# Optimization experiments

Measured on AMD Instinct MI355X. Metric: run time of the kernel, lower is better.

The kernel has to match this reference:

```python
import jax, jax.numpy as jnp
import numpy as np
import math

DIM = 512
NUM_HEADS = 8
DIM_HEAD = DIM // NUM_HEADS


def normalized_coords(h, w):
    # (h*w, 2) with (x, y) in [0, 1]
    y = jnp.linspace(0.0, 1.0, h)
    x = jnp.linspace(0.0, 1.0, w)
    yg, xg = jnp.meshgrid(y, x, indexing='ij')
    return jnp.stack([xg.ravel(), yg.ravel()], axis=-1)


def rotate_half(x):
    dh = x.shape[-1] // 2
    return jnp.concatenate([-x[..., dh:], x[..., :dh]], axis=-1)


def apply_rope(t, coords):
    # t: (n, heads, seq, dim_head); coords: (seq, 2) (identical across batch)
    dim_half = t.shape[-1] // 2
    freq = 1.0 / (10000.0 ** (jnp.arange(dim_half, dtype=jnp.float32) / dim_half))
    ang_x = coords[:, 0:1] * freq  # (seq, dim_half)
    ang_y = coords[:, 1:2] * freq
    ang = jnp.concatenate([ang_x, ang_y], axis=-1)  # (seq, dim_head)
    cos, sin = jnp.cos(ang), jnp.sin(ang)
    return t * cos + rotate_half(t) * sin


def setup_inputs() -> dict:
    key = jax.random.key(0)
    ks = jax.random.split(key, 12)
    n, Np, d, H, W = 4, 1024, DIM, 64, 64
    s = 0.02
    return {
        'local_feat': jax.random.normal(ks[0], (n, Np, d), jnp.float32),
        'global_feat': jax.random.normal(ks[1], (n, d, H, W), jnp.float32),
        'Wq': jax.random.normal(ks[2], (d, d), jnp.float32) * s,
        'bq': jnp.zeros((d,), jnp.float32),
        'Wk': jax.random.normal(ks[3], (d, d), jnp.float32) * s,
        'bk': jnp.zeros((d,), jnp.float32),
        'Wv': jax.random.normal(ks[4], (d, d), jnp.float32) * s,
        'bv': jnp.zeros((d,), jnp.float32),
        'Wg': jax.random.normal(ks[5], (d, 2 * d), jnp.float32) * s,
        'bg': jnp.zeros((d,), jnp.float32),
        'Wo': jax.random.normal(ks[6], (d, d), jnp.float32) * s,
        'bo': jnp.zeros((d,), jnp.float32),
    }


def reference(local_feat, global_feat, Wq, bq, Wk, bk, Wv, bv, Wg, bg, Wo, bo):
    n, Np, d = local_feat.shape
    _, _, H, W = global_feat.shape
    h, dh = NUM_HEADS, DIM_HEAD
    gf = global_feat.reshape(n, d, H * W).transpose(0, 2, 1)  # (n, HW, d)

    P = int(math.isqrt(Np))
    local_coords = normalized_coords(P, P)      # (Np, 2)
    global_coords = normalized_coords(H, W)     # (HW, 2)

    def proj(x, Wt, b):
        return x @ Wt.T + b

    Q = proj(local_feat, Wq, bq).reshape(n, Np, h, dh).transpose(0, 2, 1, 3)
    K = proj(gf, Wk, bk).reshape(n, H * W, h, dh).transpose(0, 2, 1, 3)
    V = proj(gf, Wv, bv).reshape(n, H * W, h, dh).transpose(0, 2, 1, 3)

    Q = apply_rope(Q, local_coords)
    K = apply_rope(K, global_coords)

    scores = jnp.einsum('bhqd,bhkd->bhqk', Q, K) / math.sqrt(dh)
    attn = jax.nn.softmax(scores, axis=-1)
    ao = jnp.einsum('bhqk,bhkd->bhqd', attn, V)
    ao = ao.transpose(0, 2, 1, 3).reshape(n, Np, d)

    gate = jax.nn.sigmoid(jnp.concatenate([local_feat, ao], axis=-1) @ Wg.T + bg)
    enhanced = local_feat + gate * ao
    return enhanced @ Wo.T + bo
```

## Files before the change

### kernel.cpp

```cpp
#include <hip/hip_runtime.h>
#include <hip/hip_bf16.h>
#include <cstdint>

typedef __hip_bfloat16 BF;
typedef unsigned short ushort_t;
typedef __attribute__((ext_vector_type(8))) __bf16 bf16x8;
typedef __attribute__((ext_vector_type(4))) float f32x4;

__device__ __forceinline__ float b2f(BF x) { return __bfloat162float(x); }
__device__ __forceinline__ unsigned short f2bu(float f) {
  union { BF b; unsigned short u; } c; c.b = __float2bfloat16(f); return c.u;
}
__device__ __forceinline__ float rdE(const void* p, size_t i, bool f32) {
  return f32 ? ((const float*)p)[i] : __bfloat162float(((const BF*)p)[i]);
}
__device__ __forceinline__ void rd16(const void* p, size_t i, bool f32, ushort_t* out) {
  if (f32) {
    const float* fp = (const float*)p + i;
#pragma unroll
    for (int j = 0; j < 16; j += 4) {
      float4 v = *(const float4*)(fp + j);
      out[j] = f2bu(v.x); out[j + 1] = f2bu(v.y);
      out[j + 2] = f2bu(v.z); out[j + 3] = f2bu(v.w);
    }
  } else {
    const uint4* up = (const uint4*)((const BF*)p + i);
    *(uint4*)&out[0] = up[0];
    *(uint4*)&out[8] = up[1];
  }
}

__global__ void detect_k(const unsigned short* __restrict__ x, int* __restrict__ flag) {
  __shared__ int cnt;
  if (threadIdx.x == 0) cnt = 0;
  __syncthreads();
  int c = 0;
  for (int i = threadIdx.x; i < 4096; i += 256) {
    int e = (x[i] >> 7) & 0xFF;
    if (e >= 0x86) c++;
  }
  if (c) atomicAdd(&cnt, c);
  __syncthreads();
  if (threadIdx.x == 0) *flag = (cnt > 64) ? 1 : 0;
}

template <int MODE>
__global__ __launch_bounds__(256) void mgemm_k(
    const void* __restrict__ Aext, const BF* __restrict__ Aint,
    const void* __restrict__ Bw, const void* __restrict__ Bw2,
    const void* __restrict__ biasv, const void* __restrict__ bias2,
    BF* __restrict__ outInt, BF* __restrict__ outInt2,
    void* __restrict__ outExt, int Kdim, const int* __restrict__ flagp) {
  const bool f32 = (*flagp != 0);
  const int tid = threadIdx.x;
  const int w = tid >> 6, lane = tid & 63;
  const int quad = lane >> 4, l16 = lane & 15;

  if constexpr (MODE == 5) {
    __shared__ __align__(16) ushort_t smem[2][128][72];
    auto As = smem[0];
    auto Bs = smem[1];
    const int wm = w >> 1, wn = w & 1;
    const int g = blockIdx.x;
    const int a = g & 7, y = (g >> 3) & 7, bidx = g >> 6;
    const int m0 = ((bidx << 1) | (a & 1)) * 128;
    const int n0 = y * 128;
    const int bz = a >> 1;

    f32x4 acc[4][4] = {};
    for (int k0 = 0; k0 < Kdim; k0 += 64) {
      __syncthreads();
#pragma unroll
      for (int u = 0; u < 2; ++u) {
        int unit = tid + u * 256;
        int k = unit >> 3, mg = unit & 7;
        int ksw = k ^ (8 * (mg & 3));
        size_t base = (size_t)bz * 512 * 4096 + (size_t)(k0 + k) * 4096 + m0 + mg * 16;
        ushort_t vals[16];
        rd16(Aext, base, f32, vals);
#pragma unroll
        for (int j = 0; j < 16; ++j) As[mg * 16 + j][ksw] = vals[j];
      }
#pragma unroll
      for (int u = 0; u < 2; ++u) {
        int unit = tid + u * 256;
        int row = unit >> 2, cg = unit & 3;
        const void* bsrc = (n0 >= 512) ? Bw2 : Bw;
        size_t nrow = (n0 >= 512) ? (n0 - 512 + row) : (n0 + row);
        ushort_t vals[16];
        rd16(bsrc, nrow * Kdim + k0 + cg * 16, f32, vals);
        *(uint4*)&Bs[row][cg * 16] = *(uint4*)&vals[0];
        *(uint4*)&Bs[row][cg * 16 + 8] = *(uint4*)&vals[8];
      }
      __syncthreads();
#pragma unroll
      for (int kc = 0; kc < 2; ++kc) {
        bf16x8 af[4], bfv[4];
#pragma unroll
        for (int i = 0; i < 4; ++i) {
          int col = (kc * 32 + quad * 8) ^ (8 * (i & 3));
          af[i] = *(const bf16x8*)&As[wm * 64 + i * 16 + l16][col];
          bfv[i] = *(const bf16x8*)&Bs[wn * 64 + i * 16 + l16][kc * 32 + quad * 8];
        }
#pragma unroll
        for (int mt = 0; mt < 4; ++mt)
#pragma unroll
          for (int nt = 0; nt < 4; ++nt)
            acc[mt][nt] = __builtin_amdgcn_mfma_f32_16x16x32_bf16(af[mt], bfv[nt], acc[mt][nt], 0, 0, 0);
      }
    }
    if (n0 < 512) {
      const int head = (n0 + wn * 64) >> 6;
#pragma unroll
      for (int mt = 0; mt < 4; ++mt)
#pragma unroll
        for (int r = 0; r < 4; ++r) {
          int pg = m0 + wm * 64 + mt * 16 + quad * 4 + r;
          float x = (float)(pg & 63) * (1.f / 63.f);
          float yy = (float)(pg >> 6) * (1.f / 63.f);
          size_t base = (((size_t)bz * 8 + head) * 4096 + pg) * 64;
#pragma unroll
          for (int j = 0; j < 2; ++j) {
            int c0 = j * 16 + l16;
            float t0 = acc[mt][j][r] + rdE(biasv, head * 64 + c0, f32);
            float t1 = acc[mt][j + 2][r] + rdE(biasv, head * 64 + c0 + 32, f32);
            float fr = __expf((float)c0 * (-9.210340371976184f / 32.f));
            float ax = x * fr, ay = yy * fr;
            outInt[base + c0] = __float2bfloat16(t0 * __cosf(ax) - t1 * __sinf(ax));
            outInt[base + c0 + 32] = __float2bfloat16(t1 * __cosf(ay) + t0 * __sinf(ay));
          }
        }
    } else {
      const int n0v = n0 - 512;
      __syncthreads();
      ushort_t (*T)[136] = (ushort_t(*)[136]) & smem[0][0][0];
#pragma unroll
      for (int mt = 0; mt < 4; ++mt)
#pragma unroll
        for (int nt = 0; nt < 4; ++nt)
#pragma unroll
          for (int r = 0; r < 4; ++r) {
            int n_l = wn * 64 + nt * 16 + l16;
            int m_l = wm * 64 + mt * 16 + quad * 4 + r;
            T[n_l][m_l] = f2bu(acc[mt][nt][r] + rdE(bias2, n0v + n_l, f32));
          }
      __syncthreads();
      int row = tid >> 1, half = tid & 1;
      size_t gbase = (((size_t)bz * 8 + (n0v >> 6) + (row >> 6)) * 64 + (row & 63)) * 4096 +
                     m0 + half * 64;
      uint4* dst = (uint4*)(outInt2 + gbase);
      const uint4* src = (const uint4*)&T[row][half * 64];
#pragma unroll
      for (int j = 0; j < 8; ++j) dst[j] = src[j];
    }
  } else {
    __shared__ __align__(16) ushort_t As[64][72];
    __shared__ __align__(16) ushort_t Bs[64][72];
    const int m0 = blockIdx.x * 64, n0 = blockIdx.y * 64;

    f32x4 acc[4] = {};
    for (int k0 = 0; k0 < Kdim; k0 += 64) {
      __syncthreads();
      {
        int row = tid >> 2, cg = tid & 3;
        int kg = k0 + cg * 16;
        ushort_t vals[16];
        if constexpr (MODE == 3) {
          if (kg < 512) {
            rd16(Aext, (size_t)(m0 + row) * 512 + kg, f32, vals);
          } else {
            const uint4* p = (const uint4*)(Aint + (size_t)(m0 + row) * 512 + (kg - 512));
            *(uint4*)&vals[0] = p[0]; *(uint4*)&vals[8] = p[1];
          }
        } else if constexpr (MODE == 4) {
          const uint4* p = (const uint4*)(Aint + (size_t)(m0 + row) * 512 + kg);
          *(uint4*)&vals[0] = p[0]; *(uint4*)&vals[8] = p[1];
        } else {
          rd16(Aext, (size_t)(m0 + row) * Kdim + kg, f32, vals);
        }
        *(uint4*)&As[row][cg * 16] = *(uint4*)&vals[0];
        *(uint4*)&As[row][cg * 16 + 8] = *(uint4*)&vals[8];
        ushort_t bv[16];
        rd16(Bw, (size_t)(n0 + row) * Kdim + kg, f32, bv);
        *(uint4*)&Bs[row][cg * 16] = *(uint4*)&bv[0];
        *(uint4*)&Bs[row][cg * 16 + 8] = *(uint4*)&bv[8];
      }
      __syncthreads();
#pragma unroll
      for (int kc = 0; kc < 2; ++kc) {
        bf16x8 af = *(const bf16x8*)&As[w * 16 + l16][kc * 32 + quad * 8];
#pragma unroll
        for (int nt = 0; nt < 4; ++nt) {
          bf16x8 bfv = *(const bf16x8*)&Bs[nt * 16 + l16][kc * 32 + quad * 8];
          acc[nt] = __builtin_amdgcn_mfma_f32_16x16x32_bf16(af, bfv, acc[nt], 0, 0, 0);
        }
      }
    }

    if constexpr (MODE == 0) {
      const int head = n0 >> 6;
#pragma unroll
      for (int r = 0; r < 4; ++r) {
        int mg = m0 + w * 16 + quad * 4 + r;
        int bb = mg >> 10, qi = mg & 1023;
        float x = (float)(qi & 31) * (1.f / 31.f);
        float y = (float)(qi >> 5) * (1.f / 31.f);
        size_t base = (((size_t)bb * 8 + head) * 1024 + qi) * 64;
#pragma unroll
        for (int j = 0; j < 2; ++j) {
          int c0 = j * 16 + l16;
          float t0 = acc[j][r] + rdE(biasv, head * 64 + c0, f32);
          float t1 = acc[j + 2][r] + rdE(biasv, head * 64 + c0 + 32, f32);
          float fr = __expf((float)c0 * (-9.210340371976184f / 32.f));
          float ax = x * fr, ay = y * fr;
          outInt[base + c0] = __float2bfloat16(t0 * __cosf(ax) - t1 * __sinf(ax));
          outInt[base + c0 + 32] = __float2bfloat16(t1 * __cosf(ay) + t0 * __sinf(ay));
        }
      }
    } else if constexpr (MODE == 3) {
#pragma unroll
      for (int r = 0; r < 4; ++r) {
        int mg = m0 + w * 16 + quad * 4 + r;
#pragma unroll
        for (int nt = 0; nt < 4; ++nt) {
          int ng = n0 + nt * 16 + l16;
          size_t idx = (size_t)mg * 512 + ng;
          float g = 1.f / (1.f + __expf(-(acc[nt][r] + rdE(biasv, ng, f32))));
          outInt[idx] = __float2bfloat16(rdE(Aext, idx, f32) + g * b2f(Aint[idx]));
        }
      }
    } else {
#pragma unroll
      for (int r = 0; r < 4; ++r) {
        int mg = m0 + w * 16 + quad * 4 + r;
#pragma unroll
        for (int nt = 0; nt < 4; ++nt) {
          int ng = n0 + nt * 16 + l16;
          size_t idx = (size_t)mg * 512 + ng;
          float v = acc[nt][r] + rdE(biasv, ng, f32);
          if (f32) ((float*)outExt)[idx] = v;
          else ((BF*)outExt)[idx] = __float2bfloat16(v);
        }
      }
    }
  }
}

template <int NS>
__global__ __launch_bounds__(256) void attn_k(const BF* __restrict__ Q,
                                              const BF* __restrict__ K,
                                              const BF* __restrict__ VT,
                                              BF* __restrict__ AO,
                                              BF* __restrict__ Opart,
                                              float* __restrict__ lpart) {
  __shared__ __align__(16) ushort_t Ks[64][72];
  __shared__ __align__(16) ushort_t VTs[64][72];
  __shared__ __align__(16) ushort_t Ps[4][32][72];

  const int tid = threadIdx.x;
  const int w = tid >> 6, lane = tid & 63;
  const int quad = lane >> 4, l16 = lane & 15;

  const int g = blockIdx.x;
  const int bh = g & 31;
  const int qt = (g >> 5) & 7;
  const int ks = g >> 8;
  const int b = bh >> 3, h = bh & 7;
  const int q0 = qt * 128 + w * 32;
  const int kspan = 4096 / NS, kbase = ks * kspan;

  bf16x8 qa[2][2];
#pragma unroll
  for (int qs = 0; qs < 2; ++qs) {
    const BF* qp = Q + (((size_t)bh << 10) + q0 + qs * 16 + l16) * 64 + quad * 8;
#pragma unroll
    for (int hh = 0; hh < 2; ++hh) {
      bf16x8 t = *(const bf16x8*)(qp + 32 * hh);
#pragma unroll
      for (int j = 0; j < 8; ++j) t[j] = (__bf16)(0.1803368801111f * (float)t[j]);
      qa[qs][hh] = t;
    }
  }

  const BF* Kp = K + (size_t)bh * 4096 * 64;
  const BF* VTp = VT + (size_t)bh * 64 * 4096;

  f32x4 o[2][4] = {};
  float lp[2][4] = {};

  const int srow = tid >> 2, scol = (tid & 3) * 16;
  {
    const uint4* kp = (const uint4*)(Kp + (size_t)(kbase + srow) * 64 + scol);
    const uint4* vp = (const uint4*)(VTp + (size_t)srow * 4096 + kbase + scol);
    uint4 a = kp[0], bb = kp[1], c = vp[0], d = vp[1];
    *(uint4*)&Ks[srow][scol] = a;  *(uint4*)&Ks[srow][scol + 8] = bb;
    *(uint4*)&VTs[srow][scol] = c; *(uint4*)&VTs[srow][scol + 8] = d;
  }

  for (int c0 = kbase; c0 < kbase + kspan; c0 += 64) {
    __syncthreads();
    uint4 nk0, nk1, nv0, nv1;
    const bool more = (c0 + 64 < kbase + kspan);
    if (more) {
      const uint4* kp = (const uint4*)(Kp + (size_t)(c0 + 64 + srow) * 64 + scol);
      const uint4* vp = (const uint4*)(VTp + (size_t)srow * 4096 + c0 + 64 + scol);
      nk0 = kp[0]; nk1 = kp[1]; nv0 = vp[0]; nv1 = vp[1];
    }

#pragma unroll
    for (int ct = 0; ct < 4; ++ct) {
      bf16x8 kb0 = *(const bf16x8*)&Ks[ct * 16 + l16][quad * 8];
      bf16x8 kb1 = *(const bf16x8*)&Ks[ct * 16 + l16][32 + quad * 8];
#pragma unroll
      for (int qs = 0; qs < 2; ++qs) {
        f32x4 s = {};
        s = __builtin_amdgcn_mfma_f32_16x16x32_bf16(qa[qs][0], kb0, s, 0, 0, 0);
        s = __builtin_amdgcn_mfma_f32_16x16x32_bf16(qa[qs][1], kb1, s, 0, 0, 0);
#pragma unroll
        for (int r = 0; r < 4; ++r) {
          float p = __builtin_exp2f(s[r]);
          lp[qs][r] += p;
          Ps[w][qs * 16 + quad * 4 + r][ct * 16 + l16] = f2bu(p);
        }
      }
    }

    bf16x8 pa[2][2];
#pragma unroll
    for (int qs = 0; qs < 2; ++qs) {
      pa[qs][0] = *(const bf16x8*)&Ps[w][qs * 16 + l16][quad * 8];
      pa[qs][1] = *(const bf16x8*)&Ps[w][qs * 16 + l16][32 + quad * 8];
    }
#pragma unroll
    for (int nt = 0; nt < 4; ++nt) {
      bf16x8 vb0 = *(const bf16x8*)&VTs[nt * 16 + l16][quad * 8];
      bf16x8 vb1 = *(const bf16x8*)&VTs[nt * 16 + l16][32 + quad * 8];
#pragma unroll
      for (int qs = 0; qs < 2; ++qs) {
        o[qs][nt] = __builtin_amdgcn_mfma_f32_16x16x32_bf16(pa[qs][0], vb0, o[qs][nt], 0, 0, 0);
        o[qs][nt] = __builtin_amdgcn_mfma_f32_16x16x32_bf16(pa[qs][1], vb1, o[qs][nt], 0, 0, 0);
      }
    }

    __syncthreads();
    if (more) {
      *(uint4*)&Ks[srow][scol] = nk0;  *(uint4*)&Ks[srow][scol + 8] = nk1;
      *(uint4*)&VTs[srow][scol] = nv0; *(uint4*)&VTs[srow][scol + 8] = nv1;
    }
  }

#pragma unroll
  for (int qs = 0; qs < 2; ++qs) {
    float invl[4];
#pragma unroll
    for (int r = 0; r < 4; ++r) {
      float v = lp[qs][r];
#pragma unroll
      for (int d = 1; d < 16; d <<= 1) v += __shfl_xor(v, d);
      if (NS == 1) invl[r] = 1.f / v;
      else if (l16 == 0)
        lpart[ks * 32768 + (bh << 10) + q0 + qs * 16 + quad * 4 + r] = v;
    }
#pragma unroll
    for (int nt = 0; nt < 4; ++nt)
#pragma unroll
      for (int r = 0; r < 4; ++r) {
        int qg = q0 + qs * 16 + quad * 4 + r;
        if (NS == 1) {
          AO[(((size_t)b << 10) + qg) * 512 + h * 64 + nt * 16 + l16] =
              __float2bfloat16(o[qs][nt][r] * invl[r]);
        } else {
          Opart[(size_t)ks * 2097152 + (((size_t)bh << 10) + qg) * 64 + nt * 16 + l16] =
              __float2bfloat16(o[qs][nt][r]);
        }
      }
  }
}

template <int NS>
__global__ __launch_bounds__(256) void reduce_k(const BF* __restrict__ Opart,
                                                const float* __restrict__ lpart,
                                                BF* __restrict__ AO) {
  int e0 = (blockIdx.x * 256 + threadIdx.x) * 4;
  int row = e0 >> 6, col = e0 & 63;
  float lsum = 0.f;
#pragma unroll
  for (int s = 0; s < NS; ++s) lsum += lpart[s * 32768 + row];
  float inv = 1.f / lsum;
  float acc[4] = {};
#pragma unroll
  for (int s = 0; s < NS; ++s) {
    uint2 u = *(const uint2*)((const ushort_t*)Opart + (size_t)s * 2097152 +
                              (size_t)row * 64 + col);
    const ushort_t* pu = (const ushort_t*)&u;
#pragma unroll
    for (int j = 0; j < 4; ++j)
      acc[j] += __uint_as_float((unsigned)pu[j] << 16);
  }
  ushort_t outv[4];
#pragma unroll
  for (int j = 0; j < 4; ++j) outv[j] = f2bu(acc[j] * inv);
  int bh = row >> 10, q = row & 1023, bb = bh >> 3, h = bh & 7;
  *(uint2*)(AO + (((size_t)bb << 10) + q) * 512 + h * 64 + col) = *(uint2*)outv;
}

extern "C" void kernel_launch(void* const* d_in, const int* in_sizes, int n_in,
                              void* d_out, int out_size, void* d_ws, size_t ws_size,
                              hipStream_t stream) {
  const void* local = d_in[0];
  const void* gfeat = d_in[1];
  const void* Wq = d_in[2];
  const void* bq = d_in[3];
  const void* Wk = d_in[4];
  const void* bk = d_in[5];
  const void* Wv = d_in[6];
  const void* bv = d_in[7];
  const void* Wg = d_in[8];
  const void* bg = d_in[9];
  const void* Wo = d_in[10];
  const void* bo = d_in[11];

  char* w = (char*)d_ws;
  int* flag = (int*)w;        w += 256;
  BF* Qb = (BF*)w;            w += (size_t)2097152 * 2;
  BF* Kb = (BF*)w;            w += (size_t)8388608 * 2;
  BF* VTb = (BF*)w;           w += (size_t)8388608 * 2;
  BF* AO = (BF*)w;            w += (size_t)2097152 * 2;
  BF* Opart = (BF*)w;
  size_t baseOff = (size_t)(w - (char*)d_ws);
  BF* ENH = Qb;

  int NS = 1;
  if (baseOff + 4 * (4194304 + 131072) <= ws_size) NS = 4;
  else if (baseOff + 2 * (4194304 + 131072) <= ws_size) NS = 2;
  float* lpart = (float*)(w + (size_t)NS * 4194304);

  dim3 blk(256);
  detect_k<<<dim3(1), blk, 0, stream>>>((const unsigned short*)local, flag);
  mgemm_k<0><<<dim3(64, 8, 1), blk, 0, stream>>>(local, nullptr, Wq, nullptr, bq, nullptr, Qb, nullptr, nullptr, 512, flag);
  mgemm_k<5><<<dim3(1024, 1, 1), blk, 0, stream>>>(gfeat, nullptr, Wk, Wv, bk, bv, Kb, VTb, nullptr, 512, flag);
  if (NS == 4) {
    attn_k<4><<<dim3(1024), blk, 0, stream>>>(Qb, Kb, VTb, AO, Opart, lpart);
    reduce_k<4><<<dim3(2048), blk, 0, stream>>>(Opart, lpart, AO);
  } else if (NS == 2) {
    attn_k<2><<<dim3(512), blk, 0, stream>>>(Qb, Kb, VTb, AO, Opart, lpart);
    reduce_k<2><<<dim3(2048), blk, 0, stream>>>(Opart, lpart, AO);
  } else {
    attn_k<1><<<dim3(256), blk, 0, stream>>>(Qb, Kb, VTb, AO, nullptr, nullptr);
  }
  mgemm_k<3><<<dim3(64, 8, 1), blk, 0, stream>>>(local, AO, Wg, nullptr, bg, nullptr, ENH, nullptr, nullptr, 1024, flag);
  mgemm_k<4><<<dim3(64, 8, 1), blk, 0, stream>>>(nullptr, ENH, Wo, nullptr, bo, nullptr, nullptr, nullptr, d_out, 512, flag);
}
```

Before: 293.7 us.

## Pre-transpose global features, fold Q scale into projection, transpose attention MFMAs

Adds a prep kernel that transposes global_feat into a row-major bf16 buffer, so the K/V projection GEMM loads A tiles as contiguous vectors instead of doing strided 16-element scatter writes into swizzled LDS. The softmax scale is folded into the Q projection epilogue, and the attention kernel swaps MFMA operand order so P is written to LDS with vector stores. Row sums now come from an MFMA against a ones vector instead of per-lane accumulation plus shuffles, and the output is written with packed vector stores. The cost is an extra kernel launch plus a 16 MB intermediate that shares workspace with Opart, and the NS=2 workspace check is adjusted to fit it.

```diff
diff --git a/kernel.cpp b/kernel.cpp
--- a/kernel.cpp
+++ b/kernel.cpp
@@ -44,6 +44,33 @@
   if (threadIdx.x == 0) *flag = (cnt > 64) ? 1 : 0;
 }
 
+__global__ __launch_bounds__(256) void prep_k(const void* __restrict__ gfeat,
+                                              BF* __restrict__ gfT,
+                                              const int* __restrict__ flagp) {
+  const bool f32 = (*flagp != 0);
+  __shared__ __align__(16) ushort_t T[64][72];
+  const int g = blockIdx.x;
+  const int bz = g & 3, mt = (g >> 2) & 63, kt = g >> 8;
+  const int t = threadIdx.x;
+  {
+    int krow = t >> 2, mg = t & 3;
+    ushort_t vals[16];
+    rd16(gfeat,
+         (size_t)bz * 512 * 4096 + (size_t)(kt * 64 + krow) * 4096 + mt * 64 + mg * 16,
+         f32, vals);
+#pragma unroll
+    for (int j = 0; j < 16; ++j) T[mg * 16 + j][krow] = vals[j];
+  }
+  __syncthreads();
+  int mrow = t >> 2, kg = t & 3;
+  uint4 a = *(const uint4*)&T[mrow][kg * 16];
+  uint4 b = *(const uint4*)&T[mrow][kg * 16 + 8];
+  size_t o = ((size_t)bz * 4096 + mt * 64 + mrow) * 512 + kt * 64 + kg * 16;
+  *(uint4*)&gfT[o] = a;
+  *(uint4*)&gfT[o + 8] = b;
+}
+
+#define QS 0.1803368801111f
 template <int MODE>
 __global__ __launch_bounds__(256) void mgemm_k(
     const void* __restrict__ Aext, const BF* __restrict__ Aint,
@@ -73,13 +100,11 @@
 #pragma unroll
       for (int u = 0; u < 2; ++u) {
         int unit = tid + u * 256;
-        int k = unit >> 3, mg = unit & 7;
-        int ksw = k ^ (8 * (mg & 3));
-        size_t base = (size_t)bz * 512 * 4096 + (size_t)(k0 + k) * 4096 + m0 + mg * 16;
-        ushort_t vals[16];
-        rd16(Aext, base, f32, vals);
-#pragma unroll
-        for (int j = 0; j < 16; ++j) As[mg * 16 + j][ksw] = vals[j];
+        int row = unit >> 2, cg = unit & 3;
+        const uint4* p = (const uint4*)(Aint + ((size_t)bz * 4096 + m0 + row) * 512 +
+                                        k0 + cg * 16);
+        *(uint4*)&As[row][cg * 16] = p[0];
+        *(uint4*)&As[row][cg * 16 + 8] = p[1];
       }
 #pragma unroll
       for (int u = 0; u < 2; ++u) {
@@ -98,8 +123,7 @@
         bf16x8 af[4], bfv[4];
 #pragma unroll
         for (int i = 0; i < 4; ++i) {
-          int col = (kc * 32 + quad * 8) ^ (8 * (i & 3));
-          af[i] = *(const bf16x8*)&As[wm * 64 + i * 16 + l16][col];
+          af[i] = *(const bf16x8*)&As[wm * 64 + i * 16 + l16][kc * 32 + quad * 8];
           bfv[i] = *(const bf16x8*)&Bs[wn * 64 + i * 16 + l16][kc * 32 + quad * 8];
         }
 #pragma unroll
@@ -213,8 +237,8 @@
           float t1 = acc[j + 2][r] + rdE(biasv, head * 64 + c0 + 32, f32);
           float fr = __expf((float)c0 * (-9.210340371976184f / 32.f));
           float ax = x * fr, ay = y * fr;
-          outInt[base + c0] = __float2bfloat16(t0 * __cosf(ax) - t1 * __sinf(ax));
-          outInt[base + c0 + 32] = __float2bfloat16(t1 * __cosf(ay) + t0 * __sinf(ay));
+          outInt[base + c0] = __float2bfloat16((t0 * __cosf(ax) - t1 * __sinf(ax)) * QS);
+          outInt[base + c0 + 32] = __float2bfloat16((t1 * __cosf(ay) + t0 * __sinf(ay)) * QS);
         }
       }
     } else if constexpr (MODE == 3) {
@@ -273,20 +297,18 @@
 #pragma unroll
   for (int qs = 0; qs < 2; ++qs) {
     const BF* qp = Q + (((size_t)bh << 10) + q0 + qs * 16 + l16) * 64 + quad * 8;
-#pragma unroll
-    for (int hh = 0; hh < 2; ++hh) {
-      bf16x8 t = *(const bf16x8*)(qp + 32 * hh);
-#pragma unroll
-      for (int j = 0; j < 8; ++j) t[j] = (__bf16)(0.1803368801111f * (float)t[j]);
-      qa[qs][hh] = t;
-    }
-  }
+    qa[qs][0] = *(const bf16x8*)qp;
+    qa[qs][1] = *(const bf16x8*)(qp + 32);
+  }
+  bf16x8 ones;
+#pragma unroll
+  for (int j = 0; j < 8; ++j) ones[j] = (__bf16)1.0f;
 
   const BF* Kp = K + (size_t)bh * 4096 * 64;
   const BF* VTp = VT + (size_t)bh * 64 * 4096;
 
   f32x4 o[2][4] = {};
-  float lp[2][4] = {};
+  f32x4 ol[2] = {};
 
   const int srow = tid >> 2, scol = (tid & 3) * 16;
   {
@@ -314,31 +336,27 @@
 #pragma unroll
       for (int qs = 0; qs < 2; ++qs) {
         f32x4 s = {};
-        s = __builtin_amdgcn_mfma_f32_16x16x32_bf16(qa[qs][0], kb0, s, 0, 0, 0);
-        s = __builtin_amdgcn_mfma_f32_16x16x32_bf16(qa[qs][1], kb1, s, 0, 0, 0);
-#pragma unroll
-        for (int r = 0; r < 4; ++r) {
-          float p = __builtin_exp2f(s[r]);
-          lp[qs][r] += p;
-          Ps[w][qs * 16 + quad * 4 + r][ct * 16 + l16] = f2bu(p);
-        }
-      }
-    }
-
-    bf16x8 pa[2][2];
+        s = __builtin_amdgcn_mfma_f32_16x16x32_bf16(kb0, qa[qs][0], s, 0, 0, 0);
+        s = __builtin_amdgcn_mfma_f32_16x16x32_bf16(kb1, qa[qs][1], s, 0, 0, 0);
+        ushort_t pv[4];
+#pragma unroll
+        for (int r = 0; r < 4; ++r) pv[r] = f2bu(__builtin_exp2f(s[r]));
+        *(uint2*)&Ps[w][qs * 16 + l16][ct * 16 + quad * 4] = *(uint2*)pv;
+      }
+    }
+
 #pragma unroll
     for (int qs = 0; qs < 2; ++qs) {
-      pa[qs][0] = *(const bf16x8*)&Ps[w][qs * 16 + l16][quad * 8];
-      pa[qs][1] = *(const bf16x8*)&Ps[w][qs * 16 + l16][32 + quad * 8];
-    }
-#pragma unroll
-    for (int nt = 0; nt < 4; ++nt) {
-      bf16x8 vb0 = *(const bf16x8*)&VTs[nt * 16 + l16][quad * 8];
-      bf16x8 vb1 = *(const bf16x8*)&VTs[nt * 16 + l16][32 + quad * 8];
-#pragma unroll
-      for (int qs = 0; qs < 2; ++qs) {
-        o[qs][nt] = __builtin_amdgcn_mfma_f32_16x16x32_bf16(pa[qs][0], vb0, o[qs][nt], 0, 0, 0);
-        o[qs][nt] = __builtin_amdgcn_mfma_f32_16x16x32_bf16(pa[qs][1], vb1, o[qs][nt], 0, 0, 0);
+      bf16x8 pa0 = *(const bf16x8*)&Ps[w][qs * 16 + l16][quad * 8];
+      bf16x8 pa1 = *(const bf16x8*)&Ps[w][qs * 16 + l16][32 + quad * 8];
+      ol[qs] = __builtin_amdgcn_mfma_f32_16x16x32_bf16(ones, pa0, ol[qs], 0, 0, 0);
+      ol[qs] = __builtin_amdgcn_mfma_f32_16x16x32_bf16(ones, pa1, ol[qs], 0, 0, 0);
+#pragma unroll
+      for (int nt = 0; nt < 4; ++nt) {
+        bf16x8 vb0 = *(const bf16x8*)&VTs[nt * 16 + l16][quad * 8];
+        bf16x8 vb1 = *(const bf16x8*)&VTs[nt * 16 + l16][32 + quad * 8];
+        o[qs][nt] = __builtin_amdgcn_mfma_f32_16x16x32_bf16(vb0, pa0, o[qs][nt], 0, 0, 0);
+        o[qs][nt] = __builtin_amdgcn_mfma_f32_16x16x32_bf16(vb1, pa1, o[qs][nt], 0, 0, 0);
       }
     }
 
@@ -351,29 +369,28 @@
 
 #pragma unroll
   for (int qs = 0; qs < 2; ++qs) {
-    float invl[4];
-#pragma unroll
-    for (int r = 0; r < 4; ++r) {
-      float v = lp[qs][r];
-#pragma unroll
-      for (int d = 1; d < 16; d <<= 1) v += __shfl_xor(v, d);
-      if (NS == 1) invl[r] = 1.f / v;
-      else if (l16 == 0)
-        lpart[ks * 32768 + (bh << 10) + q0 + qs * 16 + quad * 4 + r] = v;
-    }
-#pragma unroll
-    for (int nt = 0; nt < 4; ++nt)
-#pragma unroll
-      for (int r = 0; r < 4; ++r) {
-        int qg = q0 + qs * 16 + quad * 4 + r;
-        if (NS == 1) {
-          AO[(((size_t)b << 10) + qg) * 512 + h * 64 + nt * 16 + l16] =
-              __float2bfloat16(o[qs][nt][r] * invl[r]);
-        } else {
-          Opart[(size_t)ks * 2097152 + (((size_t)bh << 10) + qg) * 64 + nt * 16 + l16] =
-              __float2bfloat16(o[qs][nt][r]);
-        }
-      }
+    int qg = q0 + qs * 16 + l16;
+    if (NS == 1) {
+      float invl = 1.f / ol[qs][0];
+#pragma unroll
+      for (int nt = 0; nt < 4; ++nt) {
+        ushort_t ov[4];
+#pragma unroll
+        for (int r = 0; r < 4; ++r) ov[r] = f2bu(o[qs][nt][r] * invl);
+        *(uint2*)(AO + (((size_t)b << 10) + qg) * 512 + h * 64 + nt * 16 + quad * 4) =
+            *(uint2*)ov;
+      }
+    } else {
+      if (quad == 0) lpart[ks * 32768 + (bh << 10) + qg] = ol[qs][0];
+#pragma unroll
+      for (int nt = 0; nt < 4; ++nt) {
+        ushort_t ov[4];
+#pragma unroll
+        for (int r = 0; r < 4; ++r) ov[r] = f2bu(o[qs][nt][r]);
+        *(uint2*)(Opart + (size_t)ks * 2097152 + (((size_t)bh << 10) + qg) * 64 +
+                  nt * 16 + quad * 4) = *(uint2*)ov;
+      }
+    }
   }
 }
 
@@ -426,19 +443,21 @@
   BF* Kb = (BF*)w;            w += (size_t)8388608 * 2;
   BF* VTb = (BF*)w;           w += (size_t)8388608 * 2;
   BF* AO = (BF*)w;            w += (size_t)2097152 * 2;
+  BF* gfT = (BF*)w;
   BF* Opart = (BF*)w;
   size_t baseOff = (size_t)(w - (char*)d_ws);
   BF* ENH = Qb;
 
   int NS = 1;
   if (baseOff + 4 * (4194304 + 131072) <= ws_size) NS = 4;
-  else if (baseOff + 2 * (4194304 + 131072) <= ws_size) NS = 2;
+  else if (baseOff + 16777216 + 2 * 131072 <= ws_size) NS = 2;
   float* lpart = (float*)(w + (size_t)NS * 4194304);
 
   dim3 blk(256);
   detect_k<<<dim3(1), blk, 0, stream>>>((const unsigned short*)local, flag);
+  prep_k<<<dim3(2048), blk, 0, stream>>>(gfeat, gfT, flag);
   mgemm_k<0><<<dim3(64, 8, 1), blk, 0, stream>>>(local, nullptr, Wq, nullptr, bq, nullptr, Qb, nullptr, nullptr, 512, flag);
-  mgemm_k<5><<<dim3(1024, 1, 1), blk, 0, stream>>>(gfeat, nullptr, Wk, Wv, bk, bv, Kb, VTb, nullptr, 512, flag);
+  mgemm_k<5><<<dim3(1024, 1, 1), blk, 0, stream>>>(nullptr, gfT, Wk, Wv, bk, bv, Kb, VTb, nullptr, 512, flag);
   if (NS == 4) {
     attn_k<4><<<dim3(1024), blk, 0, stream>>>(Qb, Kb, VTb, AO, Opart, lpart);
     reduce_k<4><<<dim3(2048), blk, 0, stream>>>(Opart, lpart, AO);
```

New measurement: 281.6 us. -4.1%, faster.
